# Performance work log

Measured on AMD Instinct MI355X. Metric: run time of the kernel, lower is better.

Reference implementation:

```python
import jax, jax.numpy as jnp
import numpy as np

T, B, D, H = 2048, 32, 256, 256


def setup_inputs() -> dict:
    key = jax.random.key(0)
    ks = jax.random.split(key, 7)
    s = 1.0 / np.sqrt(H)
    return {
        "seq_embs": jax.random.normal(ks[0], (T, B, D), dtype=jnp.float32),
        "mask_x": jax.random.randint(ks[1], (T, B), 0, 2, dtype=jnp.int32),
        "hidden": jax.random.normal(ks[2], (B, H), dtype=jnp.float32),
        "w_ih": jax.random.uniform(ks[3], (3 * H, D), jnp.float32, -s, s),
        "w_hh": jax.random.uniform(ks[4], (3 * H, H), jnp.float32, -s, s),
        "b_ih": jax.random.uniform(ks[5], (3 * H,), jnp.float32, -s, s),
        "b_hh": jax.random.uniform(ks[6], (3 * H,), jnp.float32, -s, s),
    }


def reference(seq_embs, mask_x, hidden, w_ih, w_hh, b_ih, b_hh):
    # Precompute all input-side gate projections in one big GEMM: [T, B, 3H]
    gi_all = jnp.einsum("tbd,gd->tbg", seq_embs, w_ih) + b_ih
    mask_f = mask_x.astype(seq_embs.dtype)  # [T, B]

    def step(h, inp):
        gi, m_t = inp  # gi: [B, 3H], m_t: [B]
        gh = h @ w_hh.T + b_hh  # [B, 3H]
        i_r, i_z, i_n = jnp.split(gi, 3, axis=1)
        h_r, h_z, h_n = jnp.split(gh, 3, axis=1)
        r = jax.nn.sigmoid(i_r + h_r)
        z = jax.nn.sigmoid(i_z + h_z)
        n = jnp.tanh(i_n + r * h_n)
        h_t = (1.0 - z) * n + z * h  # GRUCell candidate hidden
        m = m_t[:, None]  # [B, 1]
        h_new = h_t * m + h * (1.0 - m)  # mask-gated state update
        return h_new, h_t * m  # output per step is masked candidate

    h_final, outputs = jax.lax.scan(step, hidden, (gi_all, mask_f))
    return outputs, h_final
```

## Files before the change

kernel.cpp:

```cpp
#include <hip/hip_runtime.h>
#include <hip/hip_bf16.h>

#define TT 2048
#define BB 32
#define DD 256
#define HH 256
#define GG 768

typedef _Float16 half2_t __attribute__((ext_vector_type(2)));

__device__ inline float fdot2(unsigned int w, unsigned int h, float acc) {
#if __has_builtin(__builtin_amdgcn_fdot2)
    return __builtin_amdgcn_fdot2(__builtin_bit_cast(half2_t, w),
                                  __builtin_bit_cast(half2_t, h), acc, false);
#else
    half2_t a = __builtin_bit_cast(half2_t, w);
    half2_t b = __builtin_bit_cast(half2_t, h);
    return acc + (float)a.x * (float)b.x + (float)a.y * (float)b.y;
#endif
}

__device__ inline void store4(float* p, float a, float b, float c, float d) {
    *(float4*)p = make_float4(a, b, c, d);
}
__device__ inline void store4(__hip_bfloat16* p, float a, float b, float c, float d) {
    p[0] = __float2bfloat16(a);
    p[1] = __float2bfloat16(b);
    p[2] = __float2bfloat16(c);
    p[3] = __float2bfloat16(d);
}
__device__ inline float ldgi(const float* p) { return *p; }
__device__ inline float ldgi(const __hip_bfloat16* p) { return __bfloat162float(*p); }

__global__ __launch_bounds__(256)
void pack_w(const float* __restrict__ w, unsigned int* __restrict__ wpk) {
    int i = blockIdx.x * 256 + threadIdx.x;
    int q = i / GG;
    int j = i - q * GG;
    float a = w[(size_t)j * DD + 2 * q];
    float b = w[(size_t)j * DD + 2 * q + 1];
    half2_t h = {(_Float16)a, (_Float16)b};
    wpk[i] = __builtin_bit_cast(unsigned int, h);
}

template <typename GiT>
__global__ __launch_bounds__(256)
void gemm_gi(const float* __restrict__ A,
             const float* __restrict__ W,
             const float* __restrict__ bias,
             GiT* __restrict__ C)
{
    __shared__ float As[32][68];
    __shared__ float Ws[32][68];
    const int tid = threadIdx.x;
    const int bm = blockIdx.y * 64;
    const int bn = blockIdx.x * 64;
    const int tm = (tid & 15) * 4;
    const int tn = (tid >> 4) * 4;
    const int r  = tid >> 3;
    const int c4 = (tid & 7) * 4;

    float acc[4][4] = {};

    for (int k0 = 0; k0 < 256; k0 += 32) {
#pragma unroll
        for (int rr = 0; rr < 64; rr += 32) {
            float4 a = *(const float4*)&A[(size_t)(bm + r + rr) * 256 + k0 + c4];
            As[c4 + 0][r + rr] = a.x;
            As[c4 + 1][r + rr] = a.y;
            As[c4 + 2][r + rr] = a.z;
            As[c4 + 3][r + rr] = a.w;
            float4 w = *(const float4*)&W[(size_t)(bn + r + rr) * 256 + k0 + c4];
            Ws[c4 + 0][r + rr] = w.x;
            Ws[c4 + 1][r + rr] = w.y;
            Ws[c4 + 2][r + rr] = w.z;
            Ws[c4 + 3][r + rr] = w.w;
        }
        __syncthreads();
#pragma unroll
        for (int kk = 0; kk < 32; ++kk) {
            float4 a = *(const float4*)&As[kk][tm];
            float4 w = *(const float4*)&Ws[kk][tn];
            float av[4] = {a.x, a.y, a.z, a.w};
            float wv[4] = {w.x, w.y, w.z, w.w};
#pragma unroll
            for (int i = 0; i < 4; ++i)
#pragma unroll
                for (int j = 0; j < 4; ++j)
                    acc[i][j] += av[i] * wv[j];
        }
        __syncthreads();
    }
#pragma unroll
    for (int i = 0; i < 4; ++i) {
        GiT* cp = C + (size_t)(bm + tm + i) * GG + bn + tn;
        store4(cp, acc[i][0] + bias[bn + tn + 0],
                   acc[i][1] + bias[bn + tn + 1],
                   acc[i][2] + bias[bn + tn + 2],
                   acc[i][3] + bias[bn + tn + 3]);
    }
}

template <typename GiT>
__global__ void
__attribute__((amdgpu_flat_work_group_size(768, 768), amdgpu_waves_per_eu(3, 3)))
gru_scan(const GiT* __restrict__ gi,
         const int* __restrict__ mask,
         const float* __restrict__ h0,
         const unsigned int* __restrict__ wpk,
         const float* __restrict__ b_hh,
         float* __restrict__ out,
         float* __restrict__ hfin)
{
    const int b = blockIdx.x;
    const int j = threadIdx.x;
    __shared__ __align__(16) _Float16 hhalf[HH];
    __shared__ float gh_lds[GG];
    __shared__ int mlds[TT];

    unsigned int w[128];
#pragma unroll
    for (int q = 0; q < 128; ++q)
        w[q] = wpk[q * GG + j];
#pragma unroll
    for (int q = 0; q < 128; ++q)
        asm volatile("" : "+v"(w[q]));

    for (int t = j; t < TT; t += GG)
        mlds[t] = mask[t * BB + b];

    float h_r = 0.f;
    if (j < HH) {
        h_r = h0[b * HH + j];
        hhalf[j] = (_Float16)h_r;
    }
    const float bhh = b_hh[j];
    __syncthreads();

    const uint4* hu4 = (const uint4*)hhalf;

    for (int t = 0; t < TT; ++t) {
        if (mlds[t]) {
            float ir = 0.f, iz = 0.f, inn = 0.f;
            if (j < HH) {
                const GiT* gtb = gi + ((size_t)t * BB + b) * GG;
                ir  = ldgi(gtb + j);
                iz  = ldgi(gtb + j + HH);
                inn = ldgi(gtb + j + 2 * HH);
            }

            float a0 = bhh, a1 = 0.f, a2 = 0.f, a3 = 0.f;
#pragma unroll
            for (int q4 = 0; q4 < 32; ++q4) {
                uint4 hv = hu4[q4];
                a0 = fdot2(w[4 * q4 + 0], hv.x, a0);
                a1 = fdot2(w[4 * q4 + 1], hv.y, a1);
                a2 = fdot2(w[4 * q4 + 2], hv.z, a2);
                a3 = fdot2(w[4 * q4 + 3], hv.w, a3);
            }
            gh_lds[j] = (a0 + a1) + (a2 + a3);
            __syncthreads();

            if (j < HH) {
                float hr = gh_lds[j];
                float hz = gh_lds[j + HH];
                float hn = gh_lds[j + 2 * HH];
                float r = 1.f / (1.f + __expf(-(ir + hr)));
                float z = 1.f / (1.f + __expf(-(iz + hz)));
                float e = __expf(2.f * (inn + r * hn));
                float n = 1.f - 2.f / (e + 1.f);
                float ht = (1.f - z) * n + z * h_r;
                out[((size_t)t * BB + b) * HH + j] = ht;
                h_r = ht;
                hhalf[j] = (_Float16)ht;
            }
            __syncthreads();
        } else {
            if (j < HH)
                out[((size_t)t * BB + b) * HH + j] = 0.f;
        }
    }
    if (j < HH) hfin[b * HH + j] = h_r;
}

extern "C" void kernel_launch(void* const* d_in, const int* in_sizes, int n_in,
                              void* d_out, int out_size, void* d_ws, size_t ws_size,
                              hipStream_t stream) {
    const float* seq  = (const float*)d_in[0];
    const int*   mask = (const int*)  d_in[1];
    const float* h0   = (const float*)d_in[2];
    const float* w_ih = (const float*)d_in[3];
    const float* w_hh = (const float*)d_in[4];
    const float* b_ih = (const float*)d_in[5];
    const float* b_hh = (const float*)d_in[6];

    float* out  = (float*)d_out;
    float* hfin = out + (size_t)TT * BB * HH;

    const size_t wpk_elems = (size_t)128 * GG;
    unsigned int* wpk = (unsigned int*)d_ws;
    const size_t gi_elems = (size_t)TT * BB * GG;
    const size_t need_f32 = wpk_elems * 4 + gi_elems * 4;

    pack_w<<<(128 * GG) / 256, 256, 0, stream>>>(w_hh, wpk);

    dim3 ggrid(GG / 64, (TT * BB) / 64);
    if (ws_size >= need_f32) {
        float* gip = (float*)d_ws + wpk_elems;
        gemm_gi<float><<<ggrid, 256, 0, stream>>>(seq, w_ih, b_ih, gip);
        gru_scan<float><<<BB, GG, 0, stream>>>(gip, mask, h0, wpk, b_hh, out, hfin);
    } else {
        __hip_bfloat16* gip = (__hip_bfloat16*)((float*)d_ws + wpk_elems);
        gemm_gi<__hip_bfloat16><<<ggrid, 256, 0, stream>>>(seq, w_ih, b_ih, gip);
        gru_scan<__hip_bfloat16><<<BB, GG, 0, stream>>>(gip, mask, h0, wpk, b_hh, out, hfin);
    }
}
```

Measured before the change: 1.787 ms.

## Use fp16 MFMA for the input-projection GEMM with larger 128x128 tiles

Replaces the scalar fp32 register-tiled GEMM that computes the input gate projections with an MFMA 16x16x32 fp16 kernel. Inputs and weights are converted to fp16 while staging into LDS, and each wave computes a 64x64 sub-tile. The goal is to cut the time of the large precompute GEMM that runs before the sequential scan. In exchange, fp16 rounding of the inputs lowers precision, and the output stores become scalar and strided per lane.

```diff
diff --git a/kernel.cpp b/kernel.cpp
--- a/kernel.cpp
+++ b/kernel.cpp
@@ -8,6 +8,8 @@
 #define GG 768
 
 typedef _Float16 half2_t __attribute__((ext_vector_type(2)));
+typedef _Float16 f16x8 __attribute__((ext_vector_type(8)));
+typedef float    f32x4 __attribute__((ext_vector_type(4)));
 
 __device__ inline float fdot2(unsigned int w, unsigned int h, float acc) {
 #if __has_builtin(__builtin_amdgcn_fdot2)
@@ -20,17 +22,10 @@
 #endif
 }
 
-__device__ inline void store4(float* p, float a, float b, float c, float d) {
-    *(float4*)p = make_float4(a, b, c, d);
-}
-__device__ inline void store4(__hip_bfloat16* p, float a, float b, float c, float d) {
-    p[0] = __float2bfloat16(a);
-    p[1] = __float2bfloat16(b);
-    p[2] = __float2bfloat16(c);
-    p[3] = __float2bfloat16(d);
-}
 __device__ inline float ldgi(const float* p) { return *p; }
 __device__ inline float ldgi(const __hip_bfloat16* p) { return __bfloat162float(*p); }
+__device__ inline void stgi(float* p, float v) { *p = v; }
+__device__ inline void stgi(__hip_bfloat16* p, float v) { *p = __float2bfloat16(v); }
 
 __global__ __launch_bounds__(256)
 void pack_w(const float* __restrict__ w, unsigned int* __restrict__ wpk) {
@@ -45,59 +40,77 @@
 
 template <typename GiT>
 __global__ __launch_bounds__(256)
-void gemm_gi(const float* __restrict__ A,
-             const float* __restrict__ W,
-             const float* __restrict__ bias,
-             GiT* __restrict__ C)
+void gemm_gi_mfma(const float* __restrict__ A,
+                  const float* __restrict__ W,
+                  const float* __restrict__ bias,
+                  GiT* __restrict__ C)
 {
-    __shared__ float As[32][68];
-    __shared__ float Ws[32][68];
+    __shared__ __align__(16) _Float16 Asl[128][40];
+    __shared__ __align__(16) _Float16 Bsl[128][40];
+
     const int tid = threadIdx.x;
-    const int bm = blockIdx.y * 64;
-    const int bn = blockIdx.x * 64;
-    const int tm = (tid & 15) * 4;
-    const int tn = (tid >> 4) * 4;
-    const int r  = tid >> 3;
-    const int c4 = (tid & 7) * 4;
-
-    float acc[4][4] = {};
-
-    for (int k0 = 0; k0 < 256; k0 += 32) {
-#pragma unroll
-        for (int rr = 0; rr < 64; rr += 32) {
-            float4 a = *(const float4*)&A[(size_t)(bm + r + rr) * 256 + k0 + c4];
-            As[c4 + 0][r + rr] = a.x;
-            As[c4 + 1][r + rr] = a.y;
-            As[c4 + 2][r + rr] = a.z;
-            As[c4 + 3][r + rr] = a.w;
-            float4 w = *(const float4*)&W[(size_t)(bn + r + rr) * 256 + k0 + c4];
-            Ws[c4 + 0][r + rr] = w.x;
-            Ws[c4 + 1][r + rr] = w.y;
-            Ws[c4 + 2][r + rr] = w.z;
-            Ws[c4 + 3][r + rr] = w.w;
+    const int wv  = tid >> 6;
+    const int l   = tid & 63;
+    const int wm  = (wv & 1) * 64;
+    const int wn  = (wv >> 1) * 64;
+    const size_t bm = (size_t)blockIdx.y * 128;
+    const int    bn = blockIdx.x * 128;
+
+    const int lr = tid >> 3;
+    const int lc = (tid & 7) * 4;
+
+    f32x4 acc[4][4] = {};
+
+    for (int kt = 0; kt < 256; kt += 32) {
+#pragma unroll
+        for (int rr = 0; rr < 128; rr += 32) {
+            float4 av = *(const float4*)&A[(bm + lr + rr) * DD + kt + lc];
+            half2_t p0 = {(_Float16)av.x, (_Float16)av.y};
+            half2_t p1 = {(_Float16)av.z, (_Float16)av.w};
+            uint2 pk = {__builtin_bit_cast(unsigned int, p0),
+                        __builtin_bit_cast(unsigned int, p1)};
+            *(uint2*)&Asl[lr + rr][lc] = pk;
+        }
+#pragma unroll
+        for (int rr = 0; rr < 128; rr += 32) {
+            float4 bv = *(const float4*)&W[(size_t)(bn + lr + rr) * DD + kt + lc];
+            half2_t p0 = {(_Float16)bv.x, (_Float16)bv.y};
+            half2_t p1 = {(_Float16)bv.z, (_Float16)bv.w};
+            uint2 pk = {__builtin_bit_cast(unsigned int, p0),
+                        __builtin_bit_cast(unsigned int, p1)};
+            *(uint2*)&Bsl[lr + rr][lc] = pk;
         }
         __syncthreads();
-#pragma unroll
-        for (int kk = 0; kk < 32; ++kk) {
-            float4 a = *(const float4*)&As[kk][tm];
-            float4 w = *(const float4*)&Ws[kk][tn];
-            float av[4] = {a.x, a.y, a.z, a.w};
-            float wv[4] = {w.x, w.y, w.z, w.w};
-#pragma unroll
-            for (int i = 0; i < 4; ++i)
-#pragma unroll
-                for (int j = 0; j < 4; ++j)
-                    acc[i][j] += av[i] * wv[j];
-        }
+
+        f16x8 af[4], bf[4];
+#pragma unroll
+        for (int i = 0; i < 4; ++i) {
+            af[i] = *(const f16x8*)&Asl[wm + i * 16 + (l & 15)][(l >> 4) * 8];
+            bf[i] = *(const f16x8*)&Bsl[wn + i * 16 + (l & 15)][(l >> 4) * 8];
+        }
+#pragma unroll
+        for (int mi = 0; mi < 4; ++mi)
+#pragma unroll
+            for (int ni = 0; ni < 4; ++ni)
+                acc[mi][ni] = __builtin_amdgcn_mfma_f32_16x16x32_f16(
+                    af[mi], bf[ni], acc[mi][ni], 0, 0, 0);
         __syncthreads();
     }
-#pragma unroll
-    for (int i = 0; i < 4; ++i) {
-        GiT* cp = C + (size_t)(bm + tm + i) * GG + bn + tn;
-        store4(cp, acc[i][0] + bias[bn + tn + 0],
-                   acc[i][1] + bias[bn + tn + 1],
-                   acc[i][2] + bias[bn + tn + 2],
-                   acc[i][3] + bias[bn + tn + 3]);
+
+    const int crow = (l >> 4) * 4;
+    const int ccol = l & 15;
+#pragma unroll
+    for (int ni = 0; ni < 4; ++ni) {
+        int n = bn + wn + ni * 16 + ccol;
+        float bs = bias[n];
+#pragma unroll
+        for (int mi = 0; mi < 4; ++mi) {
+#pragma unroll
+            for (int q = 0; q < 4; ++q) {
+                size_t m = bm + wm + mi * 16 + crow + q;
+                stgi(&C[m * GG + n], acc[mi][ni][q] + bs);
+            }
+        }
     }
 }
 
@@ -204,14 +217,14 @@
 
     pack_w<<<(128 * GG) / 256, 256, 0, stream>>>(w_hh, wpk);
 
-    dim3 ggrid(GG / 64, (TT * BB) / 64);
+    dim3 ggrid(GG / 128, (TT * BB) / 128);
     if (ws_size >= need_f32) {
         float* gip = (float*)d_ws + wpk_elems;
-        gemm_gi<float><<<ggrid, 256, 0, stream>>>(seq, w_ih, b_ih, gip);
+        gemm_gi_mfma<float><<<ggrid, 256, 0, stream>>>(seq, w_ih, b_ih, gip);
         gru_scan<float><<<BB, GG, 0, stream>>>(gip, mask, h0, wpk, b_hh, out, hfin);
     } else {
         __hip_bfloat16* gip = (__hip_bfloat16*)((float*)d_ws + wpk_elems);
-        gemm_gi<__hip_bfloat16><<<ggrid, 256, 0, stream>>>(seq, w_ih, b_ih, gip);
+        gemm_gi_mfma<__hip_bfloat16><<<ggrid, 256, 0, stream>>>(seq, w_ih, b_ih, gip);
         gru_scan<__hip_bfloat16><<<BB, GG, 0, stream>>>(gip, mask, h0, wpk, b_hh, out, hfin);
     }
 }
```

Result: faster. 1.572 ms (-12.0%).
